# Performance work log

Hardware: AMD Instinct MI355X
Metric: run time of the kernel (lower is better)

The kernel has to match this reference:

```python
import jax, jax.numpy as jnp
import numpy as np
from jax import lax

B, T, H = 128, 8192, 96


def setup_inputs() -> dict:
    key = jax.random.key(0)
    ks = jax.random.split(key, 7)
    s = 1.0 / np.sqrt(H)  # PyTorch LSTM init scale
    return {
        "x": jax.random.normal(ks[0], (B, T, 1), dtype=jnp.float32),
        "w_ih": jax.random.uniform(ks[1], (4 * H, 1), jnp.float32, -s, s),
        "w_hh": jax.random.uniform(ks[2], (4 * H, H), jnp.float32, -s, s),
        "b_ih": jax.random.uniform(ks[3], (4 * H,), jnp.float32, -s, s),
        "b_hh": jax.random.uniform(ks[4], (4 * H,), jnp.float32, -s, s),
        "w_out": jax.random.uniform(ks[5], (1, H), jnp.float32, -s, s),
        "b_out": jax.random.uniform(ks[6], (1,), jnp.float32, -s, s),
    }


def reference(x, w_ih, w_hh, b_ih, b_hh, w_out, b_out):
    # x: [B, T, 1]; single-layer batch_first LSTM, zero initial (h, c).
    Bb, Tt, _ = x.shape
    Hh = w_hh.shape[1]
    # Precompute input contribution to all gates: [T, B, 4H]
    xg = jnp.einsum("bti,gi->btg", x, w_ih) + b_ih + b_hh
    xg = jnp.transpose(xg, (1, 0, 2))

    def step(carry, g):
        h, c = carry
        gates = g + h @ w_hh.T  # [B, 4H]
        i, f, gg, o = jnp.split(gates, 4, axis=-1)  # PyTorch order: i, f, g, o
        i = jax.nn.sigmoid(i)
        f = jax.nn.sigmoid(f)
        gg = jnp.tanh(gg)
        o = jax.nn.sigmoid(o)
        c = f * c + i * gg
        h = o * jnp.tanh(c)
        return (h, c), h

    h0 = jnp.zeros((Bb, Hh), x.dtype)
    (_, _), hs = lax.scan(step, (h0, h0), xg)  # hs: [T, B, H]
    hs = jnp.transpose(hs, (1, 0, 2))  # [B, T, H]
    return hs @ w_out.T + b_out  # [B, T, 1]
```

## Files before the change

kernel.cpp:

```cpp
#include <hip/hip_runtime.h>


#define T_LEN 8192
#define H_DIM 96
#define NTHR  320
#define CHUNK 128
#define LOG2E 1.44269504f

typedef float    f32x4 __attribute__((ext_vector_type(4)));
typedef _Float16 half8 __attribute__((ext_vector_type(8)));

#define MFMA16(A, B, C)                                                        \
    __builtin_amdgcn_mfma_f32_16x16x32_f16(__builtin_bit_cast(half8, (A)),     \
                                           __builtin_bit_cast(half8, (B)),     \
                                           (C), 0, 0, 0)

__device__ __forceinline__ float sig2(float s) {
    return __builtin_amdgcn_rcpf(1.0f + __builtin_amdgcn_exp2f(-s));
}
__device__ __forceinline__ float tanh2(float sg) {
    return 1.0f - 2.0f * __builtin_amdgcn_rcpf(1.0f + __builtin_amdgcn_exp2f(sg));
}

__device__ __forceinline__ f32x4 load_afrag(const float* __restrict__ w_hh,
                                            const float* __restrict__ w_out,
                                            int mt, int kt, int m, int quad) {
    half8 f;
    if (mt < 24) {
        const int r = m & 3;
        const float scale = (r == 2) ? 2.0f * LOG2E : LOG2E;
        const int orig = r * 96 + 4 * mt + (m >> 2);
        const float* src = w_hh + orig * H_DIM + kt * 32 + quad * 8;
        #pragma unroll
        for (int jj = 0; jj < 8; ++jj) f[jj] = (_Float16)(scale * src[jj]);
    } else {
        #pragma unroll
        for (int jj = 0; jj < 8; ++jj)
            f[jj] = (m == 0) ? (_Float16)w_out[kt * 32 + quad * 8 + jj]
                             : (_Float16)0.0f;
    }
    return __builtin_bit_cast(f32x4, f);
}

__global__ __launch_bounds__(NTHR, 2) void lstm_mfma15_kernel(
    const float* __restrict__ x,
    const float* __restrict__ w_ih,
    const float* __restrict__ w_hh,
    const float* __restrict__ b_ih,
    const float* __restrict__ b_hh,
    const float* __restrict__ w_out,
    const float* __restrict__ b_out,
    float* __restrict__ y)
{
    const int tid  = threadIdx.x;
    const int wv   = tid >> 6;
    const int lane = tid & 63;
    const int m    = lane & 15;
    const int quad = lane >> 4;
    const int cc   = m & 7;
    const int bsub = m >> 3;

    __shared__ __align__(16) _Float16 h_s[2][2][H_DIM];
    __shared__ __align__(16) float    y_buf[2][2][CHUNK];
    __shared__ __align__(16) float    x_s[2][T_LEN + 8];

    {
        const float* xpair = x + (size_t)(2 * blockIdx.x) * T_LEN;
        for (int i = tid * 4; i < T_LEN; i += NTHR * 4) {
            *reinterpret_cast<f32x4*>(&x_s[0][i]) =
                *reinterpret_cast<const f32x4*>(&xpair[i]);
            *reinterpret_cast<f32x4*>(&x_s[1][i]) =
                *reinterpret_cast<const f32x4*>(&xpair[T_LEN + i]);
        }
    }

    const int mt0 = 6 * wv;
    f32x4 af00 = load_afrag(w_hh, w_out, mt0 + 0, 0, m, quad);
    f32x4 af01 = load_afrag(w_hh, w_out, mt0 + 0, 1, m, quad);
    f32x4 af02 = load_afrag(w_hh, w_out, mt0 + 0, 2, m, quad);
    f32x4 af10 = load_afrag(w_hh, w_out, mt0 + 1, 0, m, quad);
    f32x4 af11 = load_afrag(w_hh, w_out, mt0 + 1, 1, m, quad);
    f32x4 af12 = load_afrag(w_hh, w_out, mt0 + 1, 2, m, quad);
    f32x4 af20 = load_afrag(w_hh, w_out, mt0 + 2, 0, m, quad);
    f32x4 af21 = load_afrag(w_hh, w_out, mt0 + 2, 1, m, quad);
    f32x4 af22 = load_afrag(w_hh, w_out, mt0 + 2, 2, m, quad);
    f32x4 af30 = load_afrag(w_hh, w_out, mt0 + 3, 0, m, quad);
    f32x4 af31 = load_afrag(w_hh, w_out, mt0 + 3, 1, m, quad);
    f32x4 af32 = load_afrag(w_hh, w_out, mt0 + 3, 2, m, quad);
    f32x4 af40 = load_afrag(w_hh, w_out, mt0 + 4, 0, m, quad);
    f32x4 af41 = load_afrag(w_hh, w_out, mt0 + 4, 1, m, quad);
    f32x4 af42 = load_afrag(w_hh, w_out, mt0 + 4, 2, m, quad);
    f32x4 af50 = load_afrag(w_hh, w_out, mt0 + 5, 0, m, quad);
    f32x4 af51 = load_afrag(w_hh, w_out, mt0 + 5, 1, m, quad);
    f32x4 af52 = load_afrag(w_hh, w_out, mt0 + 5, 2, m, quad);
    f32x4 afy0 = {0.f, 0.f, 0.f, 0.f};
    f32x4 afy1 = {0.f, 0.f, 0.f, 0.f};
    f32x4 afy2 = {0.f, 0.f, 0.f, 0.f};
    if (wv == 4) {
        afy0 = load_afrag(w_hh, w_out, 24, 0, m, quad);
        afy1 = load_afrag(w_hh, w_out, 24, 1, m, quad);
        afy2 = load_afrag(w_hh, w_out, 24, 2, m, quad);
    }
    f32x4 zero4 = {0.f, 0.f, 0.f, 0.f};
    asm volatile("" : "+v"(af00), "+v"(af01), "+v"(af02), "+v"(af10),
                      "+v"(af11), "+v"(af12), "+v"(af20));
    asm volatile("" : "+v"(af21), "+v"(af22), "+v"(af30), "+v"(af31),
                      "+v"(af32), "+v"(af40), "+v"(af41));
    asm volatile("" : "+v"(af42), "+v"(af50), "+v"(af51), "+v"(af52),
                      "+v"(afy0), "+v"(afy1), "+v"(afy2), "+v"(zero4));

    const int sel  = (cc >= 6) ? (cc - 6) : cc;
    const int cell = (wv < 4) ? (24 * wv + 4 * sel + quad) : 0;
    const float bias_i = LOG2E * (b_ih[0 * H_DIM + cell] + b_hh[0 * H_DIM + cell]);
    const float bias_f = LOG2E * (b_ih[1 * H_DIM + cell] + b_hh[1 * H_DIM + cell]);
    const float bias_g = 2.0f * LOG2E * (b_ih[2 * H_DIM + cell] + b_hh[2 * H_DIM + cell]);
    const float bias_o = LOG2E * (b_ih[3 * H_DIM + cell] + b_hh[3 * H_DIM + cell]);
    const float wih_i  = LOG2E * w_ih[0 * H_DIM + cell];
    const float wih_f  = LOG2E * w_ih[1 * H_DIM + cell];
    const float wih_g  = 2.0f * LOG2E * w_ih[2 * H_DIM + cell];
    const float wih_o  = LOG2E * w_ih[3 * H_DIM + cell];
    const float bout   = b_out[0];
    float c = 0.f;
    if (tid < 2 * H_DIM) (&h_s[0][0][0])[tid] = (_Float16)0.0f;
    __syncthreads();

    float x_cur_next = x_s[bsub][0];

    for (int it = 0; it <= T_LEN + 1; ++it) {
        const int p = it & 1;

        if (wv < 4) {
            if (it < T_LEN) {
                const f32x4 b0 = *reinterpret_cast<const f32x4*>(&h_s[p][bsub][quad * 8]);
                const f32x4 b1 = *reinterpret_cast<const f32x4*>(&h_s[p][bsub][32 + quad * 8]);
                const f32x4 b2 = *reinterpret_cast<const f32x4*>(&h_s[p][bsub][64 + quad * 8]);
                const float x_cur = x_cur_next;
                x_cur_next = x_s[bsub][(it + 1 < T_LEN) ? (it + 1) : (T_LEN - 1)];

                f32x4 acc0 = MFMA16(af00, b0, zero4);
                f32x4 acc1 = MFMA16(af10, b0, zero4);
                f32x4 acc2 = MFMA16(af20, b0, zero4);
                f32x4 acc3 = MFMA16(af30, b0, zero4);
                f32x4 acc4 = MFMA16(af40, b0, zero4);
                f32x4 acc5 = MFMA16(af50, b0, zero4);
                acc0 = MFMA16(af01, b1, acc0);
                acc1 = MFMA16(af11, b1, acc1);
                acc2 = MFMA16(af21, b1, acc2);
                acc3 = MFMA16(af31, b1, acc3);
                acc4 = MFMA16(af41, b1, acc4);
                acc5 = MFMA16(af51, b1, acc5);
                acc0 = MFMA16(af02, b2, acc0);
                acc1 = MFMA16(af12, b2, acc1);
                acc2 = MFMA16(af22, b2, acc2);
                acc3 = MFMA16(af32, b2, acc3);
                acc4 = MFMA16(af42, b2, acc4);
                acc5 = MFMA16(af52, b2, acc5);

                f32x4 g4 = acc0;
                if (sel == 1) g4 = acc1;
                if (sel == 2) g4 = acc2;
                if (sel == 3) g4 = acc3;
                if (sel == 4) g4 = acc4;
                if (sel == 5) g4 = acc5;
                const float s0 = g4.x + fmaf(x_cur, wih_i, bias_i);
                const float s1 = g4.y + fmaf(x_cur, wih_f, bias_f);
                const float s2 = g4.z + fmaf(x_cur, wih_g, bias_g);
                const float s3 = g4.w + fmaf(x_cur, wih_o, bias_o);
                const float ig = sig2(s0);
                const float fg = sig2(s1);
                const float gg = tanh2(s2);
                const float og = sig2(s3);
                c = fmaf(fg, c, ig * gg);
                const float h = og * tanh2(2.0f * LOG2E * c);
                if (cc < 6) h_s[p ^ 1][bsub][cell] = (_Float16)h;
            }
        } else {
            if (it <= T_LEN) {
                const f32x4 b0 = *reinterpret_cast<const f32x4*>(&h_s[p][bsub][quad * 8]);
                const f32x4 b1 = *reinterpret_cast<const f32x4*>(&h_s[p][bsub][32 + quad * 8]);
                const f32x4 b2 = *reinterpret_cast<const f32x4*>(&h_s[p][bsub][64 + quad * 8]);
                f32x4 accy = MFMA16(afy0, b0, zero4);
                accy = MFMA16(afy1, b1, accy);
                accy = MFMA16(afy2, b2, accy);
                if (quad == 0 && cc == 0 && it > 0)
                    y_buf[bsub][((it - 1) >> 7) & 1][(it - 1) & (CHUNK - 1)] =
                        accy.x + bout;
            }
            if ((it & (CHUNK - 1)) == 1 && it > 1) {
                const int base = it - 1 - CHUNK;
                const int pb   = (base >> 7) & 1;
                const int bsel = lane >> 5;
                const int li   = lane & 31;
                const f32x4 v =
                    *reinterpret_cast<const f32x4*>(&y_buf[bsel][pb][li * 4]);
                float* yrow = y + (size_t)(2 * blockIdx.x + bsel) * T_LEN;
                *reinterpret_cast<f32x4*>(&yrow[base + li * 4]) = v;
            }
        }
        __syncthreads();
    }
}

extern "C" void kernel_launch(void* const* d_in, const int* in_sizes, int n_in,
                              void* d_out, int out_size, void* d_ws, size_t ws_size,
                              hipStream_t stream) {
    const float* x     = (const float*)d_in[0];
    const float* w_ih  = (const float*)d_in[1];
    const float* w_hh  = (const float*)d_in[2];
    const float* b_ih  = (const float*)d_in[3];
    const float* b_hh  = (const float*)d_in[4];
    const float* w_out = (const float*)d_in[5];
    const float* b_out = (const float*)d_in[6];
    float* y = (float*)d_out;

    const int NBLK = 64;
    lstm_mfma15_kernel<<<dim3(NBLK), dim3(NTHR), 0, stream>>>(
        x, w_ih, w_hh, b_ih, b_hh, w_out, b_out, y);
}
```

Measured before the change: 3.059 ms.

## Move output projection to VALU dot, prioritize gate waves, branchless gate select

The output-projection wave now computes the w_out dot product with scalar FMAs and cross-quad shuffles instead of three MFMAs with a mostly-zero A fragment. This frees matrix-unit issue slots for the recurrence waves. The recurrence waves raise their scheduling priority with s_setprio, and the per-lane accumulator select becomes a bit-based select tree. The h store is now unconditional, since duplicate lanes write the same value, the clamp on the next x index is dropped, and the time loop is unrolled by two. The dropped clamp risks reading x_s one element past the end on the final step, depending on how x_s is sized.

```diff
diff --git a/kernel.cpp b/kernel.cpp
--- a/kernel.cpp
+++ b/kernel.cpp
@@ -42,7 +42,7 @@
     return __builtin_bit_cast(f32x4, f);
 }
 
-__global__ __launch_bounds__(NTHR, 2) void lstm_mfma15_kernel(
+__global__ __launch_bounds__(NTHR, 2) void lstm_mfma16_kernel(
     const float* __restrict__ x,
     const float* __restrict__ w_ih,
     const float* __restrict__ w_hh,
@@ -93,24 +93,30 @@
     f32x4 af50 = load_afrag(w_hh, w_out, mt0 + 5, 0, m, quad);
     f32x4 af51 = load_afrag(w_hh, w_out, mt0 + 5, 1, m, quad);
     f32x4 af52 = load_afrag(w_hh, w_out, mt0 + 5, 2, m, quad);
-    f32x4 afy0 = {0.f, 0.f, 0.f, 0.f};
-    f32x4 afy1 = {0.f, 0.f, 0.f, 0.f};
-    f32x4 afy2 = {0.f, 0.f, 0.f, 0.f};
-    if (wv == 4) {
-        afy0 = load_afrag(w_hh, w_out, 24, 0, m, quad);
-        afy1 = load_afrag(w_hh, w_out, 24, 1, m, quad);
-        afy2 = load_afrag(w_hh, w_out, 24, 2, m, quad);
-    }
     f32x4 zero4 = {0.f, 0.f, 0.f, 0.f};
     asm volatile("" : "+v"(af00), "+v"(af01), "+v"(af02), "+v"(af10),
                       "+v"(af11), "+v"(af12), "+v"(af20));
     asm volatile("" : "+v"(af21), "+v"(af22), "+v"(af30), "+v"(af31),
                       "+v"(af32), "+v"(af40), "+v"(af41));
     asm volatile("" : "+v"(af42), "+v"(af50), "+v"(af51), "+v"(af52),
-                      "+v"(afy0), "+v"(afy1), "+v"(afy2), "+v"(zero4));
+                      "+v"(zero4));
+
+    f32x4 woa0 = {0,0,0,0}, woa1 = {0,0,0,0}, wob0 = {0,0,0,0},
+          wob1 = {0,0,0,0}, woc0 = {0,0,0,0}, woc1 = {0,0,0,0};
+    if (wv == 4) {
+        woa0 = *reinterpret_cast<const f32x4*>(&w_out[quad * 8]);
+        woa1 = *reinterpret_cast<const f32x4*>(&w_out[quad * 8 + 4]);
+        wob0 = *reinterpret_cast<const f32x4*>(&w_out[32 + quad * 8]);
+        wob1 = *reinterpret_cast<const f32x4*>(&w_out[32 + quad * 8 + 4]);
+        woc0 = *reinterpret_cast<const f32x4*>(&w_out[64 + quad * 8]);
+        woc1 = *reinterpret_cast<const f32x4*>(&w_out[64 + quad * 8 + 4]);
+    }
 
     const int sel  = (cc >= 6) ? (cc - 6) : cc;
     const int cell = (wv < 4) ? (24 * wv + 4 * sel + quad) : 0;
+    const bool s_b0 = sel & 1;
+    const bool s_b1 = (sel >> 1) & 1;
+    const bool s_b2 = (sel >> 2) & 1;
     const float bias_i = LOG2E * (b_ih[0 * H_DIM + cell] + b_hh[0 * H_DIM + cell]);
     const float bias_f = LOG2E * (b_ih[1 * H_DIM + cell] + b_hh[1 * H_DIM + cell]);
     const float bias_g = 2.0f * LOG2E * (b_ih[2 * H_DIM + cell] + b_hh[2 * H_DIM + cell]);
@@ -124,8 +130,11 @@
     if (tid < 2 * H_DIM) (&h_s[0][0][0])[tid] = (_Float16)0.0f;
     __syncthreads();
 
+    if (wv < 4) __builtin_amdgcn_s_setprio(1);
+
     float x_cur_next = x_s[bsub][0];
 
+    #pragma unroll 2
     for (int it = 0; it <= T_LEN + 1; ++it) {
         const int p = it & 1;
 
@@ -135,7 +144,7 @@
                 const f32x4 b1 = *reinterpret_cast<const f32x4*>(&h_s[p][bsub][32 + quad * 8]);
                 const f32x4 b2 = *reinterpret_cast<const f32x4*>(&h_s[p][bsub][64 + quad * 8]);
                 const float x_cur = x_cur_next;
-                x_cur_next = x_s[bsub][(it + 1 < T_LEN) ? (it + 1) : (T_LEN - 1)];
+                x_cur_next = x_s[bsub][it + 1];
 
                 f32x4 acc0 = MFMA16(af00, b0, zero4);
                 f32x4 acc1 = MFMA16(af10, b0, zero4);
@@ -156,12 +165,11 @@
                 acc4 = MFMA16(af42, b2, acc4);
                 acc5 = MFMA16(af52, b2, acc5);
 
-                f32x4 g4 = acc0;
-                if (sel == 1) g4 = acc1;
-                if (sel == 2) g4 = acc2;
-                if (sel == 3) g4 = acc3;
-                if (sel == 4) g4 = acc4;
-                if (sel == 5) g4 = acc5;
+                const f32x4 t0 = s_b0 ? acc1 : acc0;
+                const f32x4 t1 = s_b0 ? acc3 : acc2;
+                const f32x4 t2 = s_b0 ? acc5 : acc4;
+                const f32x4 g4 = s_b2 ? t2 : (s_b1 ? t1 : t0);
+
                 const float s0 = g4.x + fmaf(x_cur, wih_i, bias_i);
                 const float s1 = g4.y + fmaf(x_cur, wih_f, bias_f);
                 const float s2 = g4.z + fmaf(x_cur, wih_g, bias_g);
@@ -172,19 +180,47 @@
                 const float og = sig2(s3);
                 c = fmaf(fg, c, ig * gg);
                 const float h = og * tanh2(2.0f * LOG2E * c);
-                if (cc < 6) h_s[p ^ 1][bsub][cell] = (_Float16)h;
+                h_s[p ^ 1][bsub][cell] = (_Float16)h;
             }
         } else {
             if (it <= T_LEN) {
                 const f32x4 b0 = *reinterpret_cast<const f32x4*>(&h_s[p][bsub][quad * 8]);
                 const f32x4 b1 = *reinterpret_cast<const f32x4*>(&h_s[p][bsub][32 + quad * 8]);
                 const f32x4 b2 = *reinterpret_cast<const f32x4*>(&h_s[p][bsub][64 + quad * 8]);
-                f32x4 accy = MFMA16(afy0, b0, zero4);
-                accy = MFMA16(afy1, b1, accy);
-                accy = MFMA16(afy2, b2, accy);
-                if (quad == 0 && cc == 0 && it > 0)
+                const half8 hb0 = __builtin_bit_cast(half8, b0);
+                const half8 hb1 = __builtin_bit_cast(half8, b1);
+                const half8 hb2 = __builtin_bit_cast(half8, b2);
+                float a0 = 0.f, a1 = 0.f, a2 = 0.f;
+                a0 = fmaf((float)hb0[0], woa0.x, a0);
+                a1 = fmaf((float)hb1[0], wob0.x, a1);
+                a2 = fmaf((float)hb2[0], woc0.x, a2);
+                a0 = fmaf((float)hb0[1], woa0.y, a0);
+                a1 = fmaf((float)hb1[1], wob0.y, a1);
+                a2 = fmaf((float)hb2[1], woc0.y, a2);
+                a0 = fmaf((float)hb0[2], woa0.z, a0);
+                a1 = fmaf((float)hb1[2], wob0.z, a1);
+                a2 = fmaf((float)hb2[2], woc0.z, a2);
+                a0 = fmaf((float)hb0[3], woa0.w, a0);
+                a1 = fmaf((float)hb1[3], wob0.w, a1);
+                a2 = fmaf((float)hb2[3], woc0.w, a2);
+                a0 = fmaf((float)hb0[4], woa1.x, a0);
+                a1 = fmaf((float)hb1[4], wob1.x, a1);
+                a2 = fmaf((float)hb2[4], woc1.x, a2);
+                a0 = fmaf((float)hb0[5], woa1.y, a0);
+                a1 = fmaf((float)hb1[5], wob1.y, a1);
+                a2 = fmaf((float)hb2[5], woc1.y, a2);
+                a0 = fmaf((float)hb0[6], woa1.z, a0);
+                a1 = fmaf((float)hb1[6], wob1.z, a1);
+                a2 = fmaf((float)hb2[6], woc1.z, a2);
+                a0 = fmaf((float)hb0[7], woa1.w, a0);
+                a1 = fmaf((float)hb1[7], wob1.w, a1);
+                a2 = fmaf((float)hb2[7], woc1.w, a2);
+                float acc = a0 + a1 + a2;
+                acc += __shfl_xor(acc, 32, 64);
+                acc += __shfl_xor(acc, 16, 64);
+                if ((lane == 0 || lane == 8) && it > 0)
                     y_buf[bsub][((it - 1) >> 7) & 1][(it - 1) & (CHUNK - 1)] =
-                        accy.x + bout;
+                        acc + bout;
             }
             if ((it & (CHUNK - 1)) == 1 && it > 1) {
                 const int base = it - 1 - CHUNK;
@@ -214,6 +250,6 @@
     float* y = (float*)d_out;
 
     const int NBLK = 64;
-    lstm_mfma15_kernel<<<dim3(NBLK), dim3(NTHR), 0, stream>>>(
+    lstm_mfma16_kernel<<<dim3(NBLK), dim3(NTHR), 0, stream>>>(
         x, w_ih, w_hh, b_ih, b_hh, w_out, b_out, y);
 }
```

Measured after the change: 3.078 ms. No clear change (+0.6%).
